# Performance work log

Measured on AMD Instinct MI355X. Metric: run time of the kernel, lower is better.

Reference implementation:

```python
import jax, jax.numpy as jnp
import numpy as np

H = 1024      # hidden_dim
C = 151       # len(obj_classes)
E = 200       # embed_dim (GloVe)
DIN = 2048    # inputs_dim
T = 32        # timesteps
B = 128       # batch size (uniform packed lengths)


def setup_inputs() -> dict:
    key = jax.random.key(0)
    ks = jax.random.split(key, 8)
    sequence_tensor = jax.random.normal(ks[0], (T * B, DIN), dtype=jnp.float32) * 0.1
    labels = jax.random.randint(ks[1], (T * B,), 0, C).astype(jnp.int64)
    embed = jax.random.normal(ks[2], (C + 1, E), dtype=jnp.float32) * 0.1   # obj_embed.weight
    Wi = jax.random.normal(ks[3], (DIN + E, 6 * H), dtype=jnp.float32) * 0.02  # input_linearity
    bi = jnp.zeros((6 * H,), dtype=jnp.float32)
    Ws = jax.random.normal(ks[4], (H, 5 * H), dtype=jnp.float32) * 0.02        # state_linearity
    bs = jnp.zeros((5 * H,), dtype=jnp.float32)
    Wo = jax.random.normal(ks[5], (H, C), dtype=jnp.float32) * 0.02            # out_obj
    bo = jnp.zeros((C,), dtype=jnp.float32)
    return {"sequence_tensor": sequence_tensor, "labels": labels, "embed": embed,
            "Wi": Wi, "bi": bi, "Ws": Ws, "bs": bs, "Wo": Wo, "bo": bo,
            "batch_size": B}


def reference(sequence_tensor, embed, Wi, bi, Ws, bs, Wo, bo, labels, batch_size):
    b = int(batch_size)
    t = sequence_tensor.shape[0] // b
    x = sequence_tensor.reshape(t, b, -1)          # [T, B, DIN] packed timestep-major
    lab = labels.reshape(t, b)                     # [T, B]
    h0 = jnp.zeros((b, H), dtype=sequence_tensor.dtype)
    c0 = jnp.zeros((b, H), dtype=sequence_tensor.dtype)
    e0 = jnp.broadcast_to(embed[0], (b, E))        # 'start' embedding

    def step(carry, inp):
        h, c, pe = carry
        xt, lt = inp
        ti = jnp.concatenate([xt, pe], axis=1)     # [B, DIN+E]
        pi = ti @ Wi + bi                          # [B, 6H]
        ps = h @ Ws + bs                           # [B, 5H]

        def gate(k):
            return pi[:, k * H:(k + 1) * H] + ps[:, k * H:(k + 1) * H]

        i_g = jax.nn.sigmoid(gate(0))
        f_g = jax.nn.sigmoid(gate(1))
        m_i = jnp.tanh(gate(2))
        o_g = jax.nn.sigmoid(gate(3))
        c_new = i_g * m_i + f_g * c
        out = o_g * jnp.tanh(c_new)
        hw = jax.nn.sigmoid(gate(4))
        h_new = hw * out + (1.0 - hw) * pi[:, 5 * H:6 * H]  # highway

        pred = h_new @ Wo + bo                     # [B, C]
        nzp = jnp.argmax(pred[:, 1:], axis=1) + 1  # best non-bg class
        l2e = jnp.where(lt == 0, nzp.astype(lt.dtype), lt)
        pe_new = embed[l2e + 1]                    # feedback embedding
        return (h_new, c_new, pe_new), (pred, l2e)

    _, (dists, comms) = jax.lax.scan(step, (h0, c0, e0), (x, lab))
    return dists.reshape(t * b, C), comms.reshape(t * b)
```

## Files before the change

### kernel.cpp

```cpp
#include <hip/hip_runtime.h>
#include <math.h>

#define H    1024
#define C    151
#define E    200
#define DIN  2048
#define T    32
#define B    128
#define SIXH  (6*H)
#define FIVEH (5*H)
#define KTOT  DIN
#define NEMB  (C+1)
#define NWG   160
#define COLS  32

typedef _Float16 f16x8 __attribute__((ext_vector_type(8)));
typedef _Float16 f16x4 __attribute__((ext_vector_type(4)));
typedef float    f32x4 __attribute__((ext_vector_type(4)));

#define GLOAD_LDS16(g, l) __builtin_amdgcn_global_load_lds( \
    (const __attribute__((address_space(1))) unsigned int*)(g), \
    (__attribute__((address_space(3))) unsigned int*)(l), 16, 0, 0)

__device__ __forceinline__ void gbar(int* slots, int* epoch, int tid, int val) {
    __syncthreads();
    if (tid == 0)
        __hip_atomic_fetch_add(&slots[blockIdx.x * 16], 1,
                               __ATOMIC_RELEASE, __HIP_MEMORY_SCOPE_AGENT);
    if (blockIdx.x == 0) {
        int ok;
        do {
            int v = val;
            if (tid < NWG)
                v = __hip_atomic_load(&slots[tid * 16],
                                      __ATOMIC_RELAXED, __HIP_MEMORY_SCOPE_AGENT);
            ok = __syncthreads_and(v >= val);
            if (!ok) __builtin_amdgcn_s_sleep(1);
        } while (!ok);
        if (tid == 0)
            __hip_atomic_store(epoch, val, __ATOMIC_RELEASE, __HIP_MEMORY_SCOPE_AGENT);
    } else {
        int ok;
        do {
            int v = __hip_atomic_load(epoch, __ATOMIC_RELAXED, __HIP_MEMORY_SCOPE_AGENT);
            ok = __syncthreads_and(v >= val);
            if (!ok) __builtin_amdgcn_s_sleep(1);
        } while (!ok);
    }
    __builtin_amdgcn_fence(__ATOMIC_ACQUIRE, "agent");
}

__global__ void init_kernel(float* h, float* c, _Float16* hhi, _Float16* hlo,
                            int* eidx, int* bar) {
    int i = blockIdx.x * blockDim.x + threadIdx.x;
    if (i < B * H) {
        h[i] = 0.f; c[i] = 0.f;
        hhi[i] = (_Float16)0.f; hlo[i] = (_Float16)0.f;
    }
    if (i < B) eidx[i] = 0;
    if (i < NWG * 16 + 16) bar[i] = 0;
}

__global__ void cvt_x(const float* __restrict__ X, _Float16* __restrict__ hi,
                      _Float16* __restrict__ lo) {
    size_t i = ((size_t)blockIdx.x * 256 + threadIdx.x) * 4;
    float4 v = *(const float4*)(X + i);
    f16x4 h, l;
    h.x = (_Float16)v.x; l.x = (_Float16)(v.x - (float)h.x);
    h.y = (_Float16)v.y; l.y = (_Float16)(v.y - (float)h.y);
    h.z = (_Float16)v.z; l.z = (_Float16)(v.z - (float)h.z);
    h.w = (_Float16)v.w; l.w = (_Float16)(v.w - (float)h.w);
    *(f16x4*)(hi + i) = h;
    *(f16x4*)(lo + i) = l;
}

template<int KR, int NC>
__global__ void cvt_wT(const float* __restrict__ W, _Float16* __restrict__ hi,
                       _Float16* __restrict__ lo) {
    __shared__ float tile[32][33];
    int n0 = blockIdx.x * 32, k0 = blockIdx.y * 32;
    int tx = threadIdx.x & 31, ty = threadIdx.x >> 5;
    #pragma unroll
    for (int i = 0; i < 4; ++i) {
        int k = ty + i * 8;
        tile[k][tx] = W[(size_t)(k0 + k) * NC + n0 + tx];
    }
    __syncthreads();
    #pragma unroll
    for (int i = 0; i < 4; ++i) {
        int n = ty + i * 8;
        float v = tile[tx][n];
        _Float16 h = (_Float16)v;
        size_t o = (size_t)(n0 + n) * KR + k0 + tx;
        hi[o] = h;
        lo[o] = (_Float16)(v - (float)h);
    }
}

__global__ void cvt_woT(const float* __restrict__ Wo, float* __restrict__ WoT) {
    int k = blockIdx.x * 256 + threadIdx.x;
    for (int c = 0; c < C; ++c)
        WoT[(size_t)c * H + k] = Wo[(size_t)k * C + c];
}

__global__ void etab_kernel(const float* __restrict__ embed,
                            const float* __restrict__ Wi,
                            float* __restrict__ Etab) {
    int n = blockIdx.x * 256 + threadIdx.x;
    int k = blockIdx.y;
    const float* wp = Wi + (size_t)DIN * SIXH + n;
    const float* ep = embed + k * E;
    float acc = 0.f;
    #pragma unroll 8
    for (int e = 0; e < E; ++e)
        acc = fmaf(ep[e], wp[(size_t)e * SIXH], acc);
    Etab[(size_t)k * SIXH + n] = acc;
}

__global__ __launch_bounds__(256) void big_gemm_mfma(
    const _Float16* __restrict__ Ahi, const _Float16* __restrict__ Alo,
    const _Float16* __restrict__ Bhi, const _Float16* __restrict__ Blo,
    const float* __restrict__ bi, float* __restrict__ P)
{
    __shared__ __align__(16) _Float16 sAh[128 * 32];
    __shared__ __align__(16) _Float16 sAl[128 * 32];
    __shared__ __align__(16) _Float16 sBh[128 * 32];
    __shared__ __align__(16) _Float16 sBl[128 * 32];
    const int tid = threadIdx.x;
    const int n0 = blockIdx.x * 128;
    const int m0 = blockIdx.y * 128;
    const int lane = tid & 63, w = tid >> 6;
    const int wm = (w >> 1) * 64, wn = (w & 1) * 64;
    const int lr = lane & 15, lq = lane >> 4;

    f32x4 acc[4][4];
    #pragma unroll
    for (int i = 0; i < 4; ++i)
        #pragma unroll
        for (int j = 0; j < 4; ++j)
            acc[i][j] = (f32x4){0.f, 0.f, 0.f, 0.f};

    const int row0 = tid >> 2;
    const int kc = tid & 3;
    const int kcs = kc ^ ((row0 >> 1) & 3);
    const int sw = (lq ^ ((lr >> 1) & 3)) * 8;

    for (int k0 = 0; k0 < KTOT; k0 += 32) {
        #pragma unroll
        for (int i = 0; i < 2; ++i) {
            int row = row0 + i * 64;
            size_t ga = (size_t)(m0 + row) * KTOT + k0 + kcs * 8;
            size_t gb = (size_t)(n0 + row) * KTOT + k0 + kcs * 8;
            int loff = (i * 256 + tid) * 8;
            GLOAD_LDS16(Ahi + ga, sAh + loff);
            GLOAD_LDS16(Alo + ga, sAl + loff);
            GLOAD_LDS16(Bhi + gb, sBh + loff);
            GLOAD_LDS16(Blo + gb, sBl + loff);
        }
        __syncthreads();
        f16x8 ah[4], al[4], bh[4], bl[4];
        #pragma unroll
        for (int i = 0; i < 4; ++i) {
            ah[i] = *(const f16x8*)&sAh[(wm + i * 16 + lr) * 32 + sw];
            al[i] = *(const f16x8*)&sAl[(wm + i * 16 + lr) * 32 + sw];
            bh[i] = *(const f16x8*)&sBh[(wn + i * 16 + lr) * 32 + sw];
            bl[i] = *(const f16x8*)&sBl[(wn + i * 16 + lr) * 32 + sw];
        }
        #pragma unroll
        for (int i = 0; i < 4; ++i)
            #pragma unroll
            for (int j = 0; j < 4; ++j) {
                acc[i][j] = __builtin_amdgcn_mfma_f32_16x16x32_f16(ah[i], bh[j], acc[i][j], 0, 0, 0);
                acc[i][j] = __builtin_amdgcn_mfma_f32_16x16x32_f16(ah[i], bl[j], acc[i][j], 0, 0, 0);
                acc[i][j] = __builtin_amdgcn_mfma_f32_16x16x32_f16(al[i], bh[j], acc[i][j], 0, 0, 0);
            }
        __syncthreads();
    }
    #pragma unroll
    for (int i = 0; i < 4; ++i)
        #pragma unroll
        for (int j = 0; j < 4; ++j) {
            int gcol = n0 + wn + j * 16 + lr;
            float bv = bi[gcol];
            #pragma unroll
            for (int r = 0; r < 4; ++r) {
                int grow = m0 + wm + i * 16 + lq * 4 + r;
                P[(size_t)grow * SIXH + gcol] = acc[i][j][r] + bv;
            }
        }
}

__global__ __launch_bounds__(256, 1) void fused_loop(
    const float* __restrict__ P,
    const float* __restrict__ Etab,
    const float* __restrict__ bs,
    const _Float16* __restrict__ WsThi,
    const _Float16* __restrict__ WsTlo,
    _Float16* __restrict__ hhi,
    _Float16* __restrict__ hlo,
    float* __restrict__ ps,
    const float* __restrict__ WoT,
    const float* __restrict__ bo,
    const int* __restrict__ labels,
    float* __restrict__ dists,
    float* __restrict__ comms,
    int* bar)
{
    __shared__ __align__(16) _Float16 sBh[COLS * H];
    __shared__ __align__(16) _Float16 sBl[COLS * H];
    __shared__ __align__(16) float hs[H];
    __shared__ float vals[8];
    __shared__ int   idxs[8];
    __shared__ int   s_eidx;

    const int wg  = blockIdx.x;
    const int tid = threadIdx.x;
    const int n0  = wg * COLS;
    const int lane = tid & 63, w = tid >> 6;
    const int lr = lane & 15, lq = lane >> 4;
    int* epoch = bar + NWG * 16;

    for (int gi = tid; gi < COLS * (H / 8); gi += 256) {
        int col = gi >> 7;
        int kg  = gi & 127;
        int dst = (col * (H * 2) + kg * 16) ^ ((col & 7) << 4);
        *(f16x8*)((char*)sBh + dst) = *(const f16x8*)&WsThi[(size_t)(n0 + col) * H + kg * 8];
        *(f16x8*)((char*)sBl + dst) = *(const f16x8*)&WsTlo[(size_t)(n0 + col) * H + kg * 8];
    }

    float creg[4] = {0.f, 0.f, 0.f, 0.f};
    float bsr[4][5];
    if (wg < B) {
        #pragma unroll
        for (int jj = 0; jj < 4; ++jj)
            #pragma unroll
            for (int k = 0; k < 5; ++k)
                bsr[jj][k] = bs[k * H + jj * 256 + tid];
    }
    if (tid == 0) s_eidx = 0;
    __syncthreads();

    const int mrow0 = w * 32;
    int bval = 0;

    for (int t = 0; t < T; ++t) {
        int eidx_cur = s_eidx;

        f32x4 acc[2][2];
        #pragma unroll
        for (int i = 0; i < 2; ++i)
            #pragma unroll
            for (int j = 0; j < 2; ++j)
                acc[i][j] = (f32x4){0.f, 0.f, 0.f, 0.f};

        #pragma unroll 8
        for (int k0 = 0; k0 < H; k0 += 32) {
            f16x8 ah[2], al[2], bh[2], bl[2];
            #pragma unroll
            for (int i = 0; i < 2; ++i) {
                size_t ho = (size_t)(mrow0 + i * 16 + lr) * H + k0 + lq * 8;
                ah[i] = *(const f16x8*)&hhi[ho];
                al[i] = *(const f16x8*)&hlo[ho];
            }
            #pragma unroll
            for (int j = 0; j < 2; ++j) {
                int col = j * 16 + lr;
                int off = (col * (H * 2) + (k0 + lq * 8) * 2) ^ ((col & 7) << 4);
                bh[j] = *(const f16x8*)((const char*)sBh + off);
                bl[j] = *(const f16x8*)((const char*)sBl + off);
            }
            #pragma unroll
            for (int i = 0; i < 2; ++i)
                #pragma unroll
                for (int j = 0; j < 2; ++j) {
                    acc[i][j] = __builtin_amdgcn_mfma_f32_16x16x32_f16(ah[i], bh[j], acc[i][j], 0, 0, 0);
                    acc[i][j] = __builtin_amdgcn_mfma_f32_16x16x32_f16(ah[i], bl[j], acc[i][j], 0, 0, 0);
                    acc[i][j] = __builtin_amdgcn_mfma_f32_16x16x32_f16(al[i], bh[j], acc[i][j], 0, 0, 0);
                }
        }
        #pragma unroll
        for (int i = 0; i < 2; ++i)
            #pragma unroll
            for (int j = 0; j < 2; ++j)
                #pragma unroll
                for (int r = 0; r < 4; ++r)
                    ps[(size_t)(mrow0 + i * 16 + lq * 4 + r) * FIVEH + n0 + j * 16 + lr] = acc[i][j][r];

        float pf[4][6], pe[4][6];
        if (wg < B) {
            const float* prow = P + (size_t)(t * B + wg) * SIXH;
            const float* erow = Etab + (size_t)eidx_cur * SIXH;
            #pragma unroll
            for (int jj = 0; jj < 4; ++jj)
                #pragma unroll
                for (int k = 0; k < 6; ++k) {
                    pf[jj][k] = prow[k * H + jj * 256 + tid];
                    pe[jj][k] = erow[k * H + jj * 256 + tid];
                }
        }

        ++bval; gbar(bar, epoch, tid, bval);

        if (wg < B) {
            const int b = wg;
            const float* psr = ps + (size_t)b * FIVEH;
            #pragma unroll
            for (int jj = 0; jj < 4; ++jj) {
                int j = jj * 256 + tid;
                float gv[5];
                #pragma unroll
                for (int k = 0; k < 5; ++k)
                    gv[k] = pf[jj][k] + pe[jj][k] + psr[k * H + j] + bsr[jj][k];
                float pi5 = pf[jj][5] + pe[jj][5];
                float ig = 1.f / (1.f + expf(-gv[0]));
                float fg = 1.f / (1.f + expf(-gv[1]));
                float mi = tanhf(gv[2]);
                float og = 1.f / (1.f + expf(-gv[3]));
                float hw = 1.f / (1.f + expf(-gv[4]));
                float cn = ig * mi + fg * creg[jj];
                float out = og * tanhf(cn);
                float hn = hw * out + (1.f - hw) * pi5;
                creg[jj] = cn;
                hs[j] = hn;
                _Float16 hh = (_Float16)hn;
                hhi[(size_t)b * H + j] = hh;
                hlo[(size_t)b * H + j] = (_Float16)(hn - (float)hh);
            }
            __syncthreads();
            float predv = 0.f;
            if (tid < C) {
                const float* wp = WoT + (size_t)tid * H;
                float a0 = bo[tid], a1 = 0.f, a2 = 0.f, a3 = 0.f;
                #pragma unroll 4
                for (int k = 0; k < H; k += 4) {
                    float4 w4 = *(const float4*)&wp[k];
                    float4 h4 = *(const float4*)&hs[k];
                    a0 = fmaf(h4.x, w4.x, a0);
                    a1 = fmaf(h4.y, w4.y, a1);
                    a2 = fmaf(h4.z, w4.z, a2);
                    a3 = fmaf(h4.w, w4.w, a3);
                }
                predv = (a0 + a1) + (a2 + a3);
                dists[(size_t)(t * B + b) * C + tid] = predv;
            }
            float av = (tid >= 1 && tid < C) ? predv : -1e30f;
            int   ai = tid;
            #pragma unroll
            for (int s = 32; s > 0; s >>= 1) {
                float v2 = __shfl_down(av, s, 64);
                int   i2 = __shfl_down(ai, s, 64);
                if (v2 > av || (v2 == av && i2 < ai)) { av = v2; ai = i2; }
            }
            if (lane == 0) { vals[w] = av; idxs[w] = ai; }
            __syncthreads();
            if (tid == 0) {
                float bv2 = vals[0]; int bi2 = idxs[0];
                #pragma unroll
                for (int k = 1; k < 4; ++k)
                    if (vals[k] > bv2 || (vals[k] == bv2 && idxs[k] < bi2)) {
                        bv2 = vals[k]; bi2 = idxs[k];
                    }
                int lt = labels[t * B + b];
                int comm = (lt == 0) ? bi2 : lt;
                comms[t * B + b] = (float)comm;
                s_eidx = comm + 1;
            }
        }
        ++bval; gbar(bar, epoch, tid, bval);
    }
}

__global__ __launch_bounds__(256) void ps_mfma(
    const _Float16* __restrict__ Ahi, const _Float16* __restrict__ Alo,
    const _Float16* __restrict__ Bhi, const _Float16* __restrict__ Blo,
    float* __restrict__ ps)
{
    __shared__ __align__(16) _Float16 sAh[64 * 32];
    __shared__ __align__(16) _Float16 sAl[64 * 32];
    __shared__ __align__(16) _Float16 sBh[64 * 32];
    __shared__ __align__(16) _Float16 sBl[64 * 32];
    const int tid = threadIdx.x;
    const int n0 = blockIdx.x * 64;
    const int m0 = blockIdx.y * 64;
    const int lane = tid & 63, w = tid >> 6;
    const int wm = (w >> 1) * 32, wn = (w & 1) * 32;
    const int lr = lane & 15, lq = lane >> 4;

    f32x4 acc[2][2];
    #pragma unroll
    for (int i = 0; i < 2; ++i)
        #pragma unroll
        for (int j = 0; j < 2; ++j)
            acc[i][j] = (f32x4){0.f, 0.f, 0.f, 0.f};

    const int row = tid >> 2;
    const int kc = tid & 3;

    for (int k0 = 0; k0 < H; k0 += 32) {
        size_t ga = (size_t)(m0 + row) * H + k0 + kc * 8;
        size_t gb = (size_t)(n0 + row) * H + k0 + kc * 8;
        int loff = tid * 8;
        GLOAD_LDS16(Ahi + ga, sAh + loff);
        GLOAD_LDS16(Alo + ga, sAl + loff);
        GLOAD_LDS16(Bhi + gb, sBh + loff);
        GLOAD_LDS16(Blo + gb, sBl + loff);
        __syncthreads();
        f16x8 ah[2], al[2], bh[2], bl[2];
        #pragma unroll
        for (int i = 0; i < 2; ++i) {
            ah[i] = *(const f16x8*)&sAh[(wm + i * 16 + lr) * 32 + lq * 8];
            al[i] = *(const f16x8*)&sAl[(wm + i * 16 + lr) * 32 + lq * 8];
            bh[i] = *(const f16x8*)&sBh[(wn + i * 16 + lr) * 32 + lq * 8];
            bl[i] = *(const f16x8*)&sBl[(wn + i * 16 + lr) * 32 + lq * 8];
        }
        #pragma unroll
        for (int i = 0; i < 2; ++i)
            #pragma unroll
            for (int j = 0; j < 2; ++j) {
                acc[i][j] = __builtin_amdgcn_mfma_f32_16x16x32_f16(ah[i], bh[j], acc[i][j], 0, 0, 0);
                acc[i][j] = __builtin_amdgcn_mfma_f32_16x16x32_f16(ah[i], bl[j], acc[i][j], 0, 0, 0);
                acc[i][j] = __builtin_amdgcn_mfma_f32_16x16x32_f16(al[i], bh[j], acc[i][j], 0, 0, 0);
            }
        __syncthreads();
    }
    #pragma unroll
    for (int i = 0; i < 2; ++i)
        #pragma unroll
        for (int j = 0; j < 2; ++j) {
            int gcol = n0 + wn + j * 16 + lr;
            #pragma unroll
            for (int r = 0; r < 4; ++r) {
                int grow = m0 + wm + i * 16 + lq * 4 + r;
                ps[(size_t)grow * FIVEH + gcol] = acc[i][j][r];
            }
        }
}

__global__ void gate_kernel(const float* __restrict__ P,
                            const float* __restrict__ Etab,
                            const float* __restrict__ ps,
                            const float* __restrict__ bs,
                            const int* __restrict__ eidx,
                            float* __restrict__ h,
                            float* __restrict__ c,
                            _Float16* __restrict__ hhi,
                            _Float16* __restrict__ hlo,
                            int t) {
    int j = blockIdx.x * 256 + threadIdx.x;
    int b = blockIdx.y;
    const float* prow = P + (size_t)(t * B + b) * SIXH;
    const float* erow = Etab + (size_t)eidx[b] * SIXH;
    const float* psr  = ps + (size_t)b * FIVEH;
    float g[5];
    #pragma unroll
    for (int k = 0; k < 5; ++k) {
        int col = k * H + j;
        g[k] = prow[col] + erow[col] + psr[col] + bs[col];
    }
    float pi5 = prow[5 * H + j] + erow[5 * H + j];
    float ig = 1.f / (1.f + expf(-g[0]));
    float fg = 1.f / (1.f + expf(-g[1]));
    float mi = tanhf(g[2]);
    float og = 1.f / (1.f + expf(-g[3]));
    float hw = 1.f / (1.f + expf(-g[4]));
    float cv = c[b * H + j];
    float cn = ig * mi + fg * cv;
    float out = og * tanhf(cn);
    float hn = hw * out + (1.f - hw) * pi5;
    c[b * H + j] = cn;
    h[b * H + j] = hn;
    _Float16 hh = (_Float16)hn;
    hhi[b * H + j] = hh;
    hlo[b * H + j] = (_Float16)(hn - (float)hh);
}

__global__ void pred_kernel(const float* __restrict__ h,
                            const float* __restrict__ Wo,
                            const float* __restrict__ bo,
                            const int* __restrict__ labels,
                            float* __restrict__ dists,
                            float* __restrict__ comms,
                            int* __restrict__ eidx,
                            int t) {
    __shared__ float hsb[H];
    __shared__ float vals[256];
    __shared__ int   idxs[256];
    int tid = threadIdx.x;
    int b = blockIdx.x;
    for (int i = tid; i < H / 4; i += 256)
        *(float4*)&hsb[i * 4] = *(const float4*)&h[b * H + i * 4];
    __syncthreads();
    float pred = 0.f;
    if (tid < C) {
        pred = bo[tid];
        #pragma unroll 8
        for (int k = 0; k < H; ++k)
            pred = fmaf(hsb[k], Wo[k * C + tid], pred);
        dists[(size_t)(t * B + b) * C + tid] = pred;
    }
    vals[tid] = (tid >= 1 && tid < C) ? pred : -1e30f;
    idxs[tid] = tid;
    __syncthreads();
    for (int s = 128; s > 0; s >>= 1) {
        if (tid < s) {
            float v2 = vals[tid + s];
            int   i2 = idxs[tid + s];
            if (v2 > vals[tid] || (v2 == vals[tid] && i2 < idxs[tid])) {
                vals[tid] = v2;
                idxs[tid] = i2;
            }
        }
        __syncthreads();
    }
    if (tid == 0) {
        int nzp = idxs[0];
        int lt = labels[t * B + b];
        int comm = (lt == 0) ? nzp : lt;
        comms[t * B + b] = (float)comm;
        eidx[b] = comm + 1;
    }
}

extern "C" void kernel_launch(void* const* d_in, const int* in_sizes, int n_in,
                              void* d_out, int out_size, void* d_ws, size_t ws_size,
                              hipStream_t stream) {
    const float* X      = (const float*)d_in[0];
    const int*   labels = (const int*)  d_in[1];
    const float* embed  = (const float*)d_in[2];
    const float* Wi     = (const float*)d_in[3];
    const float* bi     = (const float*)d_in[4];
    const float* Ws     = (const float*)d_in[5];
    const float* bs     = (const float*)d_in[6];
    const float* Wo     = (const float*)d_in[7];
    const float* bo     = (const float*)d_in[8];

    char* w = (char*)d_ws;
    float* P      = (float*)w;              w += (size_t)T * B * SIXH * 4;
    float* Etab   = (float*)w;              w += (size_t)NEMB * SIXH * 4;
    float* ps     = (float*)w;              w += (size_t)B * FIVEH * 4;
    float* h      = (float*)w;              w += (size_t)B * H * 4;
    float* c      = (float*)w;              w += (size_t)B * H * 4;
    _Float16* hhi = (_Float16*)w;           w += (size_t)B * H * 2;
    _Float16* hlo = (_Float16*)w;           w += (size_t)B * H * 2;
    int* eidx     = (int*)w;                w += 512;
    int* bar      = (int*)w;                w += 16384;
    _Float16* Xhi = (_Float16*)w;           w += (size_t)T * B * KTOT * 2;
    _Float16* Xlo = (_Float16*)w;           w += (size_t)T * B * KTOT * 2;
    _Float16* WiThi = (_Float16*)w;         w += (size_t)SIXH * KTOT * 2;
    _Float16* WiTlo = (_Float16*)w;         w += (size_t)SIXH * KTOT * 2;
    _Float16* WsThi = (_Float16*)w;         w += (size_t)FIVEH * H * 2;
    _Float16* WsTlo = (_Float16*)w;         w += (size_t)FIVEH * H * 2;
    float* WoT    = (float*)Xhi;

    float* dists = (float*)d_out;
    float* comms = dists + (size_t)T * B * C;

    init_kernel<<<512, 256, 0, stream>>>(h, c, hhi, hlo, eidx, bar);
    cvt_x<<<(T * B * KTOT) / (256 * 4), 256, 0, stream>>>(X, Xhi, Xlo);
    cvt_wT<KTOT, SIXH><<<dim3(SIXH / 32, KTOT / 32), 256, 0, stream>>>(Wi, WiThi, WiTlo);
    cvt_wT<H, FIVEH><<<dim3(FIVEH / 32, H / 32), 256, 0, stream>>>(Ws, WsThi, WsTlo);
    etab_kernel<<<dim3(SIXH / 256, NEMB), 256, 0, stream>>>(embed, Wi, Etab);
    big_gemm_mfma<<<dim3(SIXH / 128, (T * B) / 128), 256, 0, stream>>>(Xhi, Xlo, WiThi, WiTlo, bi, P);
    cvt_woT<<<dim3(H / 256), 256, 0, stream>>>(Wo, WoT);

    void* args[] = {(void*)&P, (void*)&Etab, (void*)&bs, (void*)&WsThi, (void*)&WsTlo,
                    (void*)&hhi, (void*)&hlo, (void*)&ps, (void*)&WoT, (void*)&bo,
                    (void*)&labels, (void*)&dists, (void*)&comms, (void*)&bar};
    hipError_t err = hipLaunchCooperativeKernel((void*)fused_loop, dim3(NWG), dim3(256),
                                                args, 0, stream);
    if (err != hipSuccess) {
        for (int t = 0; t < T; ++t) {
            ps_mfma<<<dim3(FIVEH / 64, B / 64), 256, 0, stream>>>(hhi, hlo, WsThi, WsTlo, ps);
            gate_kernel<<<dim3(H / 256, B), 256, 0, stream>>>(P, Etab, ps, bs, eidx, h, c, hhi, hlo, t);
            pred_kernel<<<B, 256, 0, stream>>>(h, Wo, bo, labels, dists, comms, eidx, t);
        }
    }
}
```

Baseline: 2.459 ms.

## Use flat all-poll grid barrier, drop Wo transpose, add nontemporal stores

The grid barrier no longer relays through block 0 and an epoch flag. Every block now polls all per-block slots directly, with an iteration guard, which removes one hop of latency per barrier. The Wo transpose kernel is removed, and the prediction dot product reads Wo in its original layout with coalesced per-class loads across threads. Outputs and h/ps writes become nontemporal stores. The flat barrier raises atomic polling traffic (160 blocks each reading 160 slots), and the guard can silently break synchronization if it ever expires.

Result: slower. 2.530 ms (+2.9%).

```diff
diff --git a/kernel.cpp b/kernel.cpp
--- a/kernel.cpp
+++ b/kernel.cpp
@@ -13,6 +13,7 @@
 #define NEMB  (C+1)
 #define NWG   160
 #define COLS  32
+#define GUARD (1 << 20)
 
 typedef _Float16 f16x8 __attribute__((ext_vector_type(8)));
 typedef _Float16 f16x4 __attribute__((ext_vector_type(4)));
@@ -22,31 +23,20 @@
     (const __attribute__((address_space(1))) unsigned int*)(g), \
     (__attribute__((address_space(3))) unsigned int*)(l), 16, 0, 0)
 
-__device__ __forceinline__ void gbar(int* slots, int* epoch, int tid, int val) {
+__device__ __forceinline__ void gbar(int* slots, int tid, int val) {
     __syncthreads();
     if (tid == 0)
         __hip_atomic_fetch_add(&slots[blockIdx.x * 16], 1,
-                               __ATOMIC_RELEASE, __HIP_MEMORY_SCOPE_AGENT);
-    if (blockIdx.x == 0) {
-        int ok;
-        do {
-            int v = val;
-            if (tid < NWG)
-                v = __hip_atomic_load(&slots[tid * 16],
-                                      __ATOMIC_RELAXED, __HIP_MEMORY_SCOPE_AGENT);
-            ok = __syncthreads_and(v >= val);
-            if (!ok) __builtin_amdgcn_s_sleep(1);
-        } while (!ok);
-        if (tid == 0)
-            __hip_atomic_store(epoch, val, __ATOMIC_RELEASE, __HIP_MEMORY_SCOPE_AGENT);
-    } else {
-        int ok;
-        do {
-            int v = __hip_atomic_load(epoch, __ATOMIC_RELAXED, __HIP_MEMORY_SCOPE_AGENT);
-            ok = __syncthreads_and(v >= val);
-            if (!ok) __builtin_amdgcn_s_sleep(1);
-        } while (!ok);
-    }
+                               __ATOMIC_ACQ_REL, __HIP_MEMORY_SCOPE_AGENT);
+    int ok, guard = 0;
+    do {
+        int v = val;
+        if (tid < NWG)
+            v = __hip_atomic_load(&slots[tid * 16],
+                                  __ATOMIC_RELAXED, __HIP_MEMORY_SCOPE_AGENT);
+        ok = __syncthreads_and(v >= val);
+        if (!ok) __builtin_amdgcn_s_sleep(1);
+    } while (!ok && ++guard < GUARD);
     __builtin_amdgcn_fence(__ATOMIC_ACQUIRE, "agent");
 }
 
@@ -58,7 +48,7 @@
         hhi[i] = (_Float16)0.f; hlo[i] = (_Float16)0.f;
     }
     if (i < B) eidx[i] = 0;
-    if (i < NWG * 16 + 16) bar[i] = 0;
+    if (i < NWG * 16) bar[i] = 0;
 }
 
 __global__ void cvt_x(const float* __restrict__ X, _Float16* __restrict__ hi,
@@ -95,12 +85,6 @@
         hi[o] = h;
         lo[o] = (_Float16)(v - (float)h);
     }
-}
-
-__global__ void cvt_woT(const float* __restrict__ Wo, float* __restrict__ WoT) {
-    int k = blockIdx.x * 256 + threadIdx.x;
-    for (int c = 0; c < C; ++c)
-        WoT[(size_t)c * H + k] = Wo[(size_t)k * C + c];
 }
 
 __global__ void etab_kernel(const float* __restrict__ embed,
@@ -199,7 +183,7 @@
     _Float16* __restrict__ hhi,
     _Float16* __restrict__ hlo,
     float* __restrict__ ps,
-    const float* __restrict__ WoT,
+    const float* __restrict__ Wo,
     const float* __restrict__ bo,
     const int* __restrict__ labels,
     float* __restrict__ dists,
@@ -218,7 +202,6 @@
     const int n0  = wg * COLS;
     const int lane = tid & 63, w = tid >> 6;
     const int lr = lane & 15, lq = lane >> 4;
-    int* epoch = bar + NWG * 16;
 
     for (int gi = tid; gi < COLS * (H / 8); gi += 256) {
         int col = gi >> 7;
@@ -284,7 +267,8 @@
             for (int j = 0; j < 2; ++j)
                 #pragma unroll
                 for (int r = 0; r < 4; ++r)
-                    ps[(size_t)(mrow0 + i * 16 + lq * 4 + r) * FIVEH + n0 + j * 16 + lr] = acc[i][j][r];
+                    __builtin_nontemporal_store(acc[i][j][r],
+                        &ps[(size_t)(mrow0 + i * 16 + lq * 4 + r) * FIVEH + n0 + j * 16 + lr]);
 
         float pf[4][6], pe[4][6];
         if (wg < B) {
@@ -299,7 +283,7 @@
                 }
         }
 
-        ++bval; gbar(bar, epoch, tid, bval);
+        ++bval; gbar(bar, tid, bval);
 
         if (wg < B) {
             const int b = wg;
@@ -323,25 +307,18 @@
                 creg[jj] = cn;
                 hs[j] = hn;
                 _Float16 hh = (_Float16)hn;
-                hhi[(size_t)b * H + j] = hh;
-                hlo[(size_t)b * H + j] = (_Float16)(hn - (float)hh);
+                __builtin_nontemporal_store(hh, &hhi[(size_t)b * H + j]);
+                __builtin_nontemporal_store((_Float16)(hn - (float)hh), &hlo[(size_t)b * H + j]);
             }
             __syncthreads();
             float predv = 0.f;
             if (tid < C) {
-                const float* wp = WoT + (size_t)tid * H;
-                float a0 = bo[tid], a1 = 0.f, a2 = 0.f, a3 = 0.f;
-                #pragma unroll 4
-                for (int k = 0; k < H; k += 4) {
-                    float4 w4 = *(const float4*)&wp[k];
-                    float4 h4 = *(const float4*)&hs[k];
-                    a0 = fmaf(h4.x, w4.x, a0);
-                    a1 = fmaf(h4.y, w4.y, a1);
-                    a2 = fmaf(h4.z, w4.z, a2);
-                    a3 = fmaf(h4.w, w4.w, a3);
-                }
-                predv = (a0 + a1) + (a2 + a3);
-                dists[(size_t)(t * B + b) * C + tid] = predv;
+                predv = bo[tid];
+                const float* wp = Wo + tid;
+                #pragma unroll 8
+                for (int k = 0; k < H; ++k)
+                    predv = fmaf(hs[k], wp[(size_t)k * C], predv);
+                __builtin_nontemporal_store(predv, &dists[(size_t)(t * B + b) * C + tid]);
             }
             float av = (tid >= 1 && tid < C) ? predv : -1e30f;
             int   ai = tid;
@@ -362,11 +339,11 @@
                     }
                 int lt = labels[t * B + b];
                 int comm = (lt == 0) ? bi2 : lt;
-                comms[t * B + b] = (float)comm;
+                __builtin_nontemporal_store((float)comm, &comms[t * B + b]);
                 s_eidx = comm + 1;
             }
         }
-        ++bval; gbar(bar, epoch, tid, bval);
+        ++bval; gbar(bar, tid, bval);
     }
 }
 
@@ -550,7 +527,6 @@
     _Float16* WiTlo = (_Float16*)w;         w += (size_t)SIXH * KTOT * 2;
     _Float16* WsThi = (_Float16*)w;         w += (size_t)FIVEH * H * 2;
     _Float16* WsTlo = (_Float16*)w;         w += (size_t)FIVEH * H * 2;
-    float* WoT    = (float*)Xhi;
 
     float* dists = (float*)d_out;
     float* comms = dists + (size_t)T * B * C;
@@ -561,10 +537,9 @@
     cvt_wT<H, FIVEH><<<dim3(FIVEH / 32, H / 32), 256, 0, stream>>>(Ws, WsThi, WsTlo);
     etab_kernel<<<dim3(SIXH / 256, NEMB), 256, 0, stream>>>(embed, Wi, Etab);
     big_gemm_mfma<<<dim3(SIXH / 128, (T * B) / 128), 256, 0, stream>>>(Xhi, Xlo, WiThi, WiTlo, bi, P);
-    cvt_woT<<<dim3(H / 256), 256, 0, stream>>>(Wo, WoT);
 
     void* args[] = {(void*)&P, (void*)&Etab, (void*)&bs, (void*)&WsThi, (void*)&WsTlo,
-                    (void*)&hhi, (void*)&hlo, (void*)&ps, (void*)&WoT, (void*)&bo,
+                    (void*)&hhi, (void*)&hlo, (void*)&ps, (void*)&Wo, (void*)&bo,
                     (void*)&labels, (void*)&dists, (void*)&comms, (void*)&bar};
     hipError_t err = hipLaunchCooperativeKernel((void*)fused_loop, dim3(NWG), dim3(256),
                                                 args, 0, stream);
```
